# Performance work log

Hardware: AMD Instinct MI355X
Metric: run time of the kernel (lower is better)

The kernel has to match this reference:

```python
import jax, jax.numpy as jnp
import numpy as np

E = 8      # num_experts
D = 1024   # input_size
H = 1024   # hidden_size
K = 2      # top_k
B = 2
S = 1024


def setup_inputs() -> dict:
    key = jax.random.key(0)
    ks = jax.random.split(key, 5)
    x = jax.random.normal(ks[0], (B, S, D), dtype=jnp.float32)
    p = jax.random.uniform(ks[1], (B * S, K), dtype=jnp.float32)
    expert_p = p / p.sum(axis=-1, keepdims=True)            # normalized top-k gates
    expert_idxs = jax.random.randint(ks[2], (B * S, K), 0, E)
    W1 = jax.random.normal(ks[3], (E, D, 2 * H), dtype=jnp.float32) * (D ** -0.5)
    W2 = jax.random.normal(ks[4], (E, H, D), dtype=jnp.float32) * (H ** -0.5)
    return {"x": x, "expert_p": expert_p, "expert_idxs": expert_idxs, "W1": W1, "W2": W2}


def reference(x, expert_p, expert_idxs, W1, W2):
    x_shape = x.shape
    xf = x.reshape(-1, x_shape[-1])                 # [N, D]
    n_tok = xf.shape[0]
    k = expert_idxs.shape[-1]
    x_pair = jnp.repeat(xf, k, axis=0)              # [N*K, D] token replicated per expert slot
    idx = expert_idxs.reshape(-1)                   # [N*K]
    p = expert_p.reshape(-1)                        # [N*K]
    y_pair = jnp.zeros((n_tok * k, x_shape[-1]), dtype=x.dtype)
    # loop over fixed small expert count; masked dense GEMM per expert
    for e in range(W1.shape[0]):
        m = (idx == e).astype(x.dtype)[:, None]     # [N*K, 1]
        hg = (x_pair * m) @ W1[e]                   # [N*K, 2H]
        h, g = jnp.split(hg, 2, axis=-1)            # chunk(2): (h, gates)
        a = jax.nn.silu(g) * h                      # SiLU-gated GLU
        y_pair = y_pair + (a @ W2[e]) * m           # [N*K, D]
    # combine: weight each pair by its gate prob and sum over top_k slots
    y = (y_pair * p[:, None]).reshape(n_tok, k, -1).sum(axis=1)
    return y.reshape(x_shape)
```

## Files before the change

### kernel.cpp

```cpp
#include <hip/hip_runtime.h>


typedef __bf16 bf16x8 __attribute__((ext_vector_type(8)));
typedef __bf16 bf16x4 __attribute__((ext_vector_type(4)));
typedef float  f32x4  __attribute__((ext_vector_type(4)));

#define NPAIR 4096
#define NTOK  2048
#define DDIM  1024
#define HDIM  1024
#define NEXP  8

#define ORDER_I   64
#define XB_OFF    (24576)
#define W1T_OFF   (XB_OFF + 4194304)
#define W2T_OFF   (W1T_OFF + 33554432)
#define ACT_OFF   (W2T_OFF + 16777216)
#define YP_OFF    (ACT_OFF + 10485760)

__global__ void bucket_kernel(const int* __restrict__ idx, int* __restrict__ wsi) {
    __shared__ int cnt[NEXP], base[NEXP], cur[NEXP];
    const int t = threadIdx.x;
    if (t < NEXP) { cnt[t] = 0; cur[t] = 0; }
    __syncthreads();
    for (int i = t; i < NPAIR; i += 256) atomicAdd(&cnt[idx[i] & 7], 1);
    __syncthreads();
    if (t == 0) {
        int off = 0;
        for (int e = 0; e < NEXP; e++) {
            base[e] = off;
            wsi[e] = cnt[e];
            wsi[8 + e] = off;
            off += (cnt[e] + 127) & ~127;
        }
    }
    __syncthreads();
    for (int i = t; i < 5120; i += 256) wsi[ORDER_I + i] = 0;
    __syncthreads();
    for (int i = t; i < NPAIR; i += 256) {
        int e = idx[i] & 7;
        int s = atomicAdd(&cur[e], 1);
        wsi[ORDER_I + base[e] + s] = i;
    }
}

__global__ void cvtx_kernel(const float* __restrict__ x, __bf16* __restrict__ xb) {
    int i = (blockIdx.x * 256 + threadIdx.x) * 4;
    float4 v = *(const float4*)(x + i);
    bf16x4 o;
    o[0] = (__bf16)v.x; o[1] = (__bf16)v.y; o[2] = (__bf16)v.z; o[3] = (__bf16)v.w;
    *(bf16x4*)(xb + i) = o;
}

__global__ void tcvt_kernel(const float* __restrict__ src, __bf16* __restrict__ dst,
                            int R, int C) {
    __shared__ float t[32][33];
    const int tx = threadIdx.x & 31, ty = threadIdx.x >> 5;
    const float* s = src + (size_t)blockIdx.z * R * C;
    __bf16* d = dst + (size_t)blockIdx.z * R * C;
    const int r0 = blockIdx.y * 32, c0 = blockIdx.x * 32;
#pragma unroll
    for (int j = 0; j < 4; j++)
        t[ty + j * 8][tx] = s[(size_t)(r0 + ty + j * 8) * C + c0 + tx];
    __syncthreads();
#pragma unroll
    for (int j = 0; j < 4; j++)
        d[(size_t)(c0 + ty + j * 8) * R + r0 + tx] = (__bf16)t[tx][ty + j * 8];
}

__global__ __launch_bounds__(256) void gemm1_kernel(const __bf16* __restrict__ xb,
                                                    const __bf16* __restrict__ w1t,
                                                    const int* __restrict__ wsi,
                                                    __bf16* __restrict__ act) {
    const int e = blockIdx.z;
    const int cnt = wsi[e];
    const int m0 = blockIdx.y * 128;
    if (m0 >= cnt) return;
    const int base = wsi[8 + e];
    const int n0 = blockIdx.x * 64;
    const int* order = wsi + ORDER_I;
    const __bf16* w1e = w1t + (size_t)e * 2048 * 1024;

    __shared__ __bf16 As[128][40];
    __shared__ __bf16 Bs[128][40];

    const int tid = threadIdx.x;
    const int lane = tid & 63, w = tid >> 6;
    const int lm = lane & 15, q = lane >> 4;

    f32x4 acc[2][8];
#pragma unroll
    for (int mt = 0; mt < 2; mt++)
#pragma unroll
        for (int nt = 0; nt < 8; nt++) acc[mt][nt] = (f32x4){0.f, 0.f, 0.f, 0.f};

    for (int k0 = 0; k0 < DDIM; k0 += 32) {
        __syncthreads();
#pragma unroll
        for (int i = 0; i < 2; i++) {
            int c = tid + i * 256;
            int row = c >> 2, ks = (c & 3) * 8;
            int m = m0 + row;
            int oi = (m < cnt) ? (base + m) : base;
            int tok = order[oi] >> 1;
            bf16x8 va = *(const bf16x8*)(xb + (size_t)tok * DDIM + k0 + ks);
            *(bf16x8*)(&As[row][ks]) = va;
            int rb = (row < 64) ? (n0 + row) : (HDIM + n0 + (row - 64));
            bf16x8 vb = *(const bf16x8*)(w1e + (size_t)rb * DDIM + k0 + ks);
            *(bf16x8*)(&Bs[row][ks]) = vb;
        }
        __syncthreads();
        bf16x8 a0 = *(const bf16x8*)(&As[w * 32 + lm][q * 8]);
        bf16x8 a1 = *(const bf16x8*)(&As[w * 32 + 16 + lm][q * 8]);
#pragma unroll
        for (int nt = 0; nt < 8; nt++) {
            bf16x8 b = *(const bf16x8*)(&Bs[nt * 16 + lm][q * 8]);
            acc[0][nt] = __builtin_amdgcn_mfma_f32_16x16x32_bf16(a0, b, acc[0][nt], 0, 0, 0);
            acc[1][nt] = __builtin_amdgcn_mfma_f32_16x16x32_bf16(a1, b, acc[1][nt], 0, 0, 0);
        }
    }
#pragma unroll
    for (int mt = 0; mt < 2; mt++)
#pragma unroll
        for (int nt = 0; nt < 4; nt++)
#pragma unroll
            for (int r = 0; r < 4; r++) {
                int m = w * 32 + mt * 16 + q * 4 + r;
                if (m0 + m < cnt) {
                    float h = acc[mt][nt][r];
                    float g = acc[mt][nt + 4][r];
                    float a = h * (g / (1.f + __expf(-g)));
                    act[(size_t)(base + m0 + m) * HDIM + n0 + nt * 16 + lm] = (__bf16)a;
                }
            }
}

__global__ __launch_bounds__(256) void gemm2_kernel(const __bf16* __restrict__ act,
                                                    const __bf16* __restrict__ w2t,
                                                    const int* __restrict__ wsi,
                                                    float* __restrict__ yp) {
    const int e = blockIdx.z;
    const int cnt = wsi[e];
    const int m0 = blockIdx.y * 128;
    if (m0 >= cnt) return;
    const int base = wsi[8 + e];
    const int n0 = blockIdx.x * 128;
    const int* order = wsi + ORDER_I;
    const __bf16* w2e = w2t + (size_t)e * 1024 * 1024;

    __shared__ __bf16 As[128][40];
    __shared__ __bf16 Bs[128][40];

    const int tid = threadIdx.x;
    const int lane = tid & 63, w = tid >> 6;
    const int lm = lane & 15, q = lane >> 4;

    f32x4 acc[2][8];
#pragma unroll
    for (int mt = 0; mt < 2; mt++)
#pragma unroll
        for (int nt = 0; nt < 8; nt++) acc[mt][nt] = (f32x4){0.f, 0.f, 0.f, 0.f};

    for (int k0 = 0; k0 < HDIM; k0 += 32) {
        __syncthreads();
#pragma unroll
        for (int i = 0; i < 2; i++) {
            int c = tid + i * 256;
            int row = c >> 2, ks = (c & 3) * 8;
            int m = m0 + row;
            int ar = (m < cnt) ? (base + m) : base;
            bf16x8 va = *(const bf16x8*)(act + (size_t)ar * HDIM + k0 + ks);
            *(bf16x8*)(&As[row][ks]) = va;
            bf16x8 vb = *(const bf16x8*)(w2e + (size_t)(n0 + row) * HDIM + k0 + ks);
            *(bf16x8*)(&Bs[row][ks]) = vb;
        }
        __syncthreads();
        bf16x8 a0 = *(const bf16x8*)(&As[w * 32 + lm][q * 8]);
        bf16x8 a1 = *(const bf16x8*)(&As[w * 32 + 16 + lm][q * 8]);
#pragma unroll
        for (int nt = 0; nt < 8; nt++) {
            bf16x8 b = *(const bf16x8*)(&Bs[nt * 16 + lm][q * 8]);
            acc[0][nt] = __builtin_amdgcn_mfma_f32_16x16x32_bf16(a0, b, acc[0][nt], 0, 0, 0);
            acc[1][nt] = __builtin_amdgcn_mfma_f32_16x16x32_bf16(a1, b, acc[1][nt], 0, 0, 0);
        }
    }
#pragma unroll
    for (int mt = 0; mt < 2; mt++)
#pragma unroll
        for (int nt = 0; nt < 8; nt++)
#pragma unroll
            for (int r = 0; r < 4; r++) {
                int m = w * 32 + mt * 16 + q * 4 + r;
                int gm = m0 + m;
                if (gm < cnt) {
                    int pi = order[base + gm];
                    yp[(size_t)pi * DDIM + n0 + nt * 16 + lm] = acc[mt][nt][r];
                }
            }
}

__global__ void combine_kernel(const float* __restrict__ yp, const float* __restrict__ p,
                               float* __restrict__ out) {
    int id = blockIdx.x * 256 + threadIdx.x;
    int n = id >> 8;
    int c = (id & 255) << 2;
    const float4 v0 = *(const float4*)(yp + (size_t)(2 * n) * DDIM + c);
    const float4 v1 = *(const float4*)(yp + (size_t)(2 * n + 1) * DDIM + c);
    float p0 = p[2 * n], p1 = p[2 * n + 1];
    float4 o;
    o.x = p0 * v0.x + p1 * v1.x;
    o.y = p0 * v0.y + p1 * v1.y;
    o.z = p0 * v0.z + p1 * v1.z;
    o.w = p0 * v0.w + p1 * v1.w;
    *(float4*)(out + (size_t)n * DDIM + c) = o;
}

extern "C" void kernel_launch(void* const* d_in, const int* in_sizes, int n_in,
                              void* d_out, int out_size, void* d_ws, size_t ws_size,
                              hipStream_t stream) {
    (void)in_sizes; (void)n_in; (void)out_size; (void)ws_size;
    const float* x   = (const float*)d_in[0];
    const float* p   = (const float*)d_in[1];
    const int* eidx  = (const int*)d_in[2];
    const float* W1  = (const float*)d_in[3];
    const float* W2  = (const float*)d_in[4];
    float* out = (float*)d_out;

    char* ws = (char*)d_ws;
    int* wsi     = (int*)ws;
    __bf16* xb   = (__bf16*)(ws + XB_OFF);
    __bf16* w1t  = (__bf16*)(ws + W1T_OFF);
    __bf16* w2t  = (__bf16*)(ws + W2T_OFF);
    __bf16* act  = (__bf16*)(ws + ACT_OFF);
    float* yp    = (float*)(ws + YP_OFF);

    bucket_kernel<<<1, 256, 0, stream>>>(eidx, wsi);
    cvtx_kernel<<<(NTOK * DDIM) / (256 * 4), 256, 0, stream>>>(x, xb);
    tcvt_kernel<<<dim3(64, 32, NEXP), 256, 0, stream>>>(W1, w1t, DDIM, 2 * HDIM);
    tcvt_kernel<<<dim3(32, 32, NEXP), 256, 0, stream>>>(W2, w2t, HDIM, DDIM);
    gemm1_kernel<<<dim3(16, 32, NEXP), 256, 0, stream>>>(xb, w1t, wsi, act);
    gemm2_kernel<<<dim3(8, 32, NEXP), 256, 0, stream>>>(act, w2t, wsi, yp);
    combine_kernel<<<NTOK, 256, 0, stream>>>(yp, p, out);
}
```

Measured before the change: 249.5 us.

## Use direct global-to-LDS loads, 2x2 wave tiling, and vectorized weight transpose

Both expert GEMMs now stage A and B tiles with global_load_lds builtins that write straight into unpadded LDS, using per-thread row pointers precomputed outside the K loop. Waves are arranged 2x2 with 4x4 MFMA tiles so each A and B fragment is reused more. The weight transpose/convert kernel moves to 64x64 tiles with float4 loads and bf16x4 stores. Removing the LDS padding may add bank conflicts on fragment reads, and the K loop still has no double buffering.

```diff
diff --git a/kernel.cpp b/kernel.cpp
--- a/kernel.cpp
+++ b/kernel.cpp
@@ -17,6 +17,11 @@
 #define W2T_OFF   (W1T_OFF + 33554432)
 #define ACT_OFF   (W2T_OFF + 16777216)
 #define YP_OFF    (ACT_OFF + 10485760)
+
+#define GLOAD_LDS16(g, l) \
+    __builtin_amdgcn_global_load_lds( \
+        (const __attribute__((address_space(1))) void*)(g), \
+        (__attribute__((address_space(3))) void*)(l), 16, 0, 0)
 
 __global__ void bucket_kernel(const int* __restrict__ idx, int* __restrict__ wsi) {
     __shared__ int cnt[NEXP], base[NEXP], cur[NEXP];
@@ -52,20 +57,31 @@
     *(bf16x4*)(xb + i) = o;
 }
 
-__global__ void tcvt_kernel(const float* __restrict__ src, __bf16* __restrict__ dst,
-                            int R, int C) {
-    __shared__ float t[32][33];
-    const int tx = threadIdx.x & 31, ty = threadIdx.x >> 5;
+__global__ __launch_bounds__(256) void tcvt_kernel(const float* __restrict__ src,
+                                                   __bf16* __restrict__ dst,
+                                                   int R, int C) {
+    __shared__ float t[64][65];
+    const int tid = threadIdx.x;
     const float* s = src + (size_t)blockIdx.z * R * C;
     __bf16* d = dst + (size_t)blockIdx.z * R * C;
-    const int r0 = blockIdx.y * 32, c0 = blockIdx.x * 32;
-#pragma unroll
-    for (int j = 0; j < 4; j++)
-        t[ty + j * 8][tx] = s[(size_t)(r0 + ty + j * 8) * C + c0 + tx];
-    __syncthreads();
-#pragma unroll
-    for (int j = 0; j < 4; j++)
-        d[(size_t)(c0 + ty + j * 8) * R + r0 + tx] = (__bf16)t[tx][ty + j * 8];
+    const int r0 = blockIdx.y * 64, c0 = blockIdx.x * 64;
+    const int lr = tid >> 4;
+    const int lc = (tid & 15) * 4;
+#pragma unroll
+    for (int p = 0; p < 4; p++) {
+        int r = p * 16 + lr;
+        float4 v = *(const float4*)(s + (size_t)(r0 + r) * C + c0 + lc);
+        t[r][lc] = v.x; t[r][lc + 1] = v.y; t[r][lc + 2] = v.z; t[r][lc + 3] = v.w;
+    }
+    __syncthreads();
+#pragma unroll
+    for (int p = 0; p < 4; p++) {
+        int c = p * 16 + lr;
+        bf16x4 o;
+#pragma unroll
+        for (int i = 0; i < 4; i++) o[i] = (__bf16)t[lc + i][c];
+        *(bf16x4*)(d + (size_t)(c0 + c) * R + r0 + lc) = o;
+    }
 }
 
 __global__ __launch_bounds__(256) void gemm1_kernel(const __bf16* __restrict__ xb,
@@ -81,58 +97,76 @@
     const int* order = wsi + ORDER_I;
     const __bf16* w1e = w1t + (size_t)e * 2048 * 1024;
 
-    __shared__ __bf16 As[128][40];
-    __shared__ __bf16 Bs[128][40];
+    __shared__ __align__(16) __bf16 As[128][32];
+    __shared__ __align__(16) __bf16 Bs[128][32];
 
     const int tid = threadIdx.x;
     const int lane = tid & 63, w = tid >> 6;
     const int lm = lane & 15, q = lane >> 4;
-
-    f32x4 acc[2][8];
-#pragma unroll
-    for (int mt = 0; mt < 2; mt++)
-#pragma unroll
-        for (int nt = 0; nt < 8; nt++) acc[mt][nt] = (f32x4){0.f, 0.f, 0.f, 0.f};
+    const int wm = w & 1, wn = w >> 1;
+
+    const __bf16* ga[2];
+    const __bf16* gb[2];
+#pragma unroll
+    for (int j = 0; j < 2; j++) {
+        int c = j * 256 + tid;
+        int r = c >> 2, ks = (c & 3) * 8;
+        int m = m0 + r; if (m >= cnt) m = cnt - 1;
+        int tok = order[base + m] >> 1;
+        ga[j] = xb + (size_t)tok * DDIM + ks;
+        int half = r >> 6, rr = r & 63;
+        int rb = (rr < 32) ? (n0 + half * 32 + rr)
+                           : (HDIM + n0 + half * 32 + (rr - 32));
+        gb[j] = w1e + (size_t)rb * DDIM + ks;
+    }
+
+    f32x4 acc[4][4];
+#pragma unroll
+    for (int mt = 0; mt < 4; mt++)
+#pragma unroll
+        for (int nt = 0; nt < 4; nt++) acc[mt][nt] = (f32x4){0.f, 0.f, 0.f, 0.f};
 
     for (int k0 = 0; k0 < DDIM; k0 += 32) {
         __syncthreads();
 #pragma unroll
-        for (int i = 0; i < 2; i++) {
-            int c = tid + i * 256;
-            int row = c >> 2, ks = (c & 3) * 8;
-            int m = m0 + row;
-            int oi = (m < cnt) ? (base + m) : base;
-            int tok = order[oi] >> 1;
-            bf16x8 va = *(const bf16x8*)(xb + (size_t)tok * DDIM + k0 + ks);
-            *(bf16x8*)(&As[row][ks]) = va;
-            int rb = (row < 64) ? (n0 + row) : (HDIM + n0 + (row - 64));
-            bf16x8 vb = *(const bf16x8*)(w1e + (size_t)rb * DDIM + k0 + ks);
-            *(bf16x8*)(&Bs[row][ks]) = vb;
-        }
-        __syncthreads();
-        bf16x8 a0 = *(const bf16x8*)(&As[w * 32 + lm][q * 8]);
-        bf16x8 a1 = *(const bf16x8*)(&As[w * 32 + 16 + lm][q * 8]);
-#pragma unroll
-        for (int nt = 0; nt < 8; nt++) {
-            bf16x8 b = *(const bf16x8*)(&Bs[nt * 16 + lm][q * 8]);
-            acc[0][nt] = __builtin_amdgcn_mfma_f32_16x16x32_bf16(a0, b, acc[0][nt], 0, 0, 0);
-            acc[1][nt] = __builtin_amdgcn_mfma_f32_16x16x32_bf16(a1, b, acc[1][nt], 0, 0, 0);
-        }
-    }
-#pragma unroll
-    for (int mt = 0; mt < 2; mt++)
-#pragma unroll
-        for (int nt = 0; nt < 4; nt++)
+        for (int j = 0; j < 2; j++) {
+            int c = j * 256 + tid;
+            GLOAD_LDS16(ga[j], (char*)&As[0][0] + c * 16);
+            GLOAD_LDS16(gb[j], (char*)&Bs[0][0] + c * 16);
+            ga[j] += 32; gb[j] += 32;
+        }
+        __syncthreads();
+        bf16x8 af[4];
+#pragma unroll
+        for (int mt = 0; mt < 4; mt++)
+            af[mt] = *(const bf16x8*)(&As[wm * 64 + mt * 16 + lm][q * 8]);
+#pragma unroll
+        for (int nt = 0; nt < 4; nt++) {
+            bf16x8 b = *(const bf16x8*)(&Bs[wn * 64 + nt * 16 + lm][q * 8]);
+#pragma unroll
+            for (int mt = 0; mt < 4; mt++)
+                acc[mt][nt] = __builtin_amdgcn_mfma_f32_16x16x32_bf16(af[mt], b, acc[mt][nt], 0, 0, 0);
+        }
+    }
+
+#pragma unroll
+    for (int mt = 0; mt < 4; mt++) {
+        int mbase = m0 + wm * 64 + mt * 16 + q * 4;
+#pragma unroll
+        for (int ntp = 0; ntp < 2; ntp++) {
+            int col = n0 + wn * 32 + ntp * 16 + lm;
 #pragma unroll
             for (int r = 0; r < 4; r++) {
-                int m = w * 32 + mt * 16 + q * 4 + r;
-                if (m0 + m < cnt) {
-                    float h = acc[mt][nt][r];
-                    float g = acc[mt][nt + 4][r];
+                int m = mbase + r;
+                if (m < cnt) {
+                    float h = acc[mt][ntp][r];
+                    float g = acc[mt][ntp + 2][r];
                     float a = h * (g / (1.f + __expf(-g)));
-                    act[(size_t)(base + m0 + m) * HDIM + n0 + nt * 16 + lm] = (__bf16)a;
+                    act[(size_t)(base + m) * HDIM + col] = (__bf16)a;
                 }
             }
+        }
+    }
 }
 
 __global__ __launch_bounds__(256) void gemm2_kernel(const __bf16* __restrict__ act,
@@ -148,55 +182,72 @@
     const int* order = wsi + ORDER_I;
     const __bf16* w2e = w2t + (size_t)e * 1024 * 1024;
 
-    __shared__ __bf16 As[128][40];
-    __shared__ __bf16 Bs[128][40];
+    __shared__ __align__(16) __bf16 As[128][32];
+    __shared__ __align__(16) __bf16 Bs[128][32];
 
     const int tid = threadIdx.x;
     const int lane = tid & 63, w = tid >> 6;
     const int lm = lane & 15, q = lane >> 4;
-
-    f32x4 acc[2][8];
-#pragma unroll
-    for (int mt = 0; mt < 2; mt++)
-#pragma unroll
-        for (int nt = 0; nt < 8; nt++) acc[mt][nt] = (f32x4){0.f, 0.f, 0.f, 0.f};
+    const int wm = w & 1, wn = w >> 1;
+
+    const __bf16* ga[2];
+    const __bf16* gb[2];
+#pragma unroll
+    for (int j = 0; j < 2; j++) {
+        int c = j * 256 + tid;
+        int r = c >> 2, ks = (c & 3) * 8;
+        ga[j] = act + (size_t)(base + m0 + r) * HDIM + ks;
+        gb[j] = w2e + (size_t)(n0 + r) * HDIM + ks;
+    }
+
+    f32x4 acc[4][4];
+#pragma unroll
+    for (int mt = 0; mt < 4; mt++)
+#pragma unroll
+        for (int nt = 0; nt < 4; nt++) acc[mt][nt] = (f32x4){0.f, 0.f, 0.f, 0.f};
 
     for (int k0 = 0; k0 < HDIM; k0 += 32) {
         __syncthreads();
 #pragma unroll
-        for (int i = 0; i < 2; i++) {
-            int c = tid + i * 256;
-            int row = c >> 2, ks = (c & 3) * 8;
-            int m = m0 + row;
-            int ar = (m < cnt) ? (base + m) : base;
-            bf16x8 va = *(const bf16x8*)(act + (size_t)ar * HDIM + k0 + ks);
-            *(bf16x8*)(&As[row][ks]) = va;
-            bf16x8 vb = *(const bf16x8*)(w2e + (size_t)(n0 + row) * HDIM + k0 + ks);
-            *(bf16x8*)(&Bs[row][ks]) = vb;
-        }
-        __syncthreads();
-        bf16x8 a0 = *(const bf16x8*)(&As[w * 32 + lm][q * 8]);
-        bf16x8 a1 = *(const bf16x8*)(&As[w * 32 + 16 + lm][q * 8]);
-#pragma unroll
-        for (int nt = 0; nt < 8; nt++) {
-            bf16x8 b = *(const bf16x8*)(&Bs[nt * 16 + lm][q * 8]);
-            acc[0][nt] = __builtin_amdgcn_mfma_f32_16x16x32_bf16(a0, b, acc[0][nt], 0, 0, 0);
-            acc[1][nt] = __builtin_amdgcn_mfma_f32_16x16x32_bf16(a1, b, acc[1][nt], 0, 0, 0);
-        }
-    }
-#pragma unroll
-    for (int mt = 0; mt < 2; mt++)
-#pragma unroll
-        for (int nt = 0; nt < 8; nt++)
+        for (int j = 0; j < 2; j++) {
+            int c = j * 256 + tid;
+            GLOAD_LDS16(ga[j], (char*)&As[0][0] + c * 16);
+            GLOAD_LDS16(gb[j], (char*)&Bs[0][0] + c * 16);
+            ga[j] += 32; gb[j] += 32;
+        }
+        __syncthreads();
+        bf16x8 af[4];
+#pragma unroll
+        for (int mt = 0; mt < 4; mt++)
+            af[mt] = *(const bf16x8*)(&As[wm * 64 + mt * 16 + lm][q * 8]);
+#pragma unroll
+        for (int nt = 0; nt < 4; nt++) {
+            bf16x8 b = *(const bf16x8*)(&Bs[wn * 64 + nt * 16 + lm][q * 8]);
+#pragma unroll
+            for (int mt = 0; mt < 4; mt++)
+                acc[mt][nt] = __builtin_amdgcn_mfma_f32_16x16x32_bf16(af[mt], b, acc[mt][nt], 0, 0, 0);
+        }
+    }
+
+    int pi[4][4];
+#pragma unroll
+    for (int mt = 0; mt < 4; mt++)
+#pragma unroll
+        for (int r = 0; r < 4; r++) {
+            int gm = m0 + wm * 64 + mt * 16 + q * 4 + r;
+            pi[mt][r] = (gm < cnt) ? order[base + gm] : -1;
+        }
+#pragma unroll
+    for (int mt = 0; mt < 4; mt++)
+#pragma unroll
+        for (int nt = 0; nt < 4; nt++) {
+            int col = n0 + wn * 64 + nt * 16 + lm;
 #pragma unroll
             for (int r = 0; r < 4; r++) {
-                int m = w * 32 + mt * 16 + q * 4 + r;
-                int gm = m0 + m;
-                if (gm < cnt) {
-                    int pi = order[base + gm];
-                    yp[(size_t)pi * DDIM + n0 + nt * 16 + lm] = acc[mt][nt][r];
-                }
+                if (pi[mt][r] >= 0)
+                    yp[(size_t)pi[mt][r] * DDIM + col] = acc[mt][nt][r];
             }
+        }
 }
 
 __global__ void combine_kernel(const float* __restrict__ yp, const float* __restrict__ p,
@@ -236,8 +287,8 @@
 
     bucket_kernel<<<1, 256, 0, stream>>>(eidx, wsi);
     cvtx_kernel<<<(NTOK * DDIM) / (256 * 4), 256, 0, stream>>>(x, xb);
-    tcvt_kernel<<<dim3(64, 32, NEXP), 256, 0, stream>>>(W1, w1t, DDIM, 2 * HDIM);
-    tcvt_kernel<<<dim3(32, 32, NEXP), 256, 0, stream>>>(W2, w2t, HDIM, DDIM);
+    tcvt_kernel<<<dim3(32, 16, NEXP), 256, 0, stream>>>(W1, w1t, DDIM, 2 * HDIM);
+    tcvt_kernel<<<dim3(16, 16, NEXP), 256, 0, stream>>>(W2, w2t, HDIM, DDIM);
     gemm1_kernel<<<dim3(16, 32, NEXP), 256, 0, stream>>>(xb, w1t, wsi, act);
     gemm2_kernel<<<dim3(8, 32, NEXP), 256, 0, stream>>>(act, w2t, wsi, yp);
     combine_kernel<<<NTOK, 256, 0, stream>>>(yp, p, out);
```

New measurement: 227.0 us. 1.1x faster.
